# Performance work log

Hardware: AMD Instinct MI355X
Metric: run time of the kernel (lower is better)

## Reference

```python
import jax, jax.numpy as jnp
import numpy as np

# MXInt config (mirrors q_config in init_kwargs)
A_MW, A_EW = 8, 4   # matmul input A mantissa/exponent widths
B_MW, B_EW = 8, 4   # matmul input B
O_MW, O_EW = 8, 4   # matmul output
SM_MW, SM_EW = 8, 4 # softmax output


def _dequant(m, e, mw):
    # m: [..., S, D] integer-valued mantissas; e: [..., S] shared row exponent
    # value = m * 2^(e - mw + 1)
    return m * jnp.exp2(e.astype(m.dtype)[..., None] - (mw - 1))


def _quant(x, mw, ew):
    # MXInt block quantization with exponent shared over the last dim.
    amax = jnp.max(jnp.abs(x), axis=-1)
    e = jnp.floor(jnp.log2(jnp.maximum(amax, jnp.exp2(jnp.float32(-126)))))
    e = jnp.clip(e, -(2 ** (ew - 1)), 2 ** (ew - 1) - 1)
    m = jnp.round(x * jnp.exp2(-(e[..., None] - (mw - 1))))
    m = jnp.clip(m, -(2 ** (mw - 1)), 2 ** (mw - 1) - 1)
    return m, e


def setup_inputs() -> dict:
    key = jax.random.key(0)
    ks = jax.random.split(key, 6)
    B, S, D = 256, 512, 64
    mquery = jax.random.randint(ks[0], (B, S, D), 0, 128).astype(jnp.float32)
    mkey = jax.random.randint(ks[1], (B, S, D), 0, 128).astype(jnp.float32)
    mvalue = jax.random.randint(ks[2], (B, S, D), 0, 128).astype(jnp.float32)
    equery = jax.random.randint(ks[3], (B, S), 0, 6, dtype=jnp.int32)
    ekey = jax.random.randint(ks[4], (B, S), 0, 6, dtype=jnp.int32)
    evalue = jax.random.randint(ks[5], (B, S), 0, 6, dtype=jnp.int32)
    return {"mquery": mquery, "equery": equery, "mkey": mkey,
            "ekey": ekey, "mvalue": mvalue, "evalue": evalue}


def reference(mquery, equery, mkey, ekey, mvalue, evalue):
    # QK^T in dequantized domain, then requantize output to MXInt (per-row exp)
    q = _dequant(mquery, equery, A_MW)            # [B,S,D]
    k = _dequant(mkey, ekey, B_MW)                # [B,S,D]
    scores = jnp.einsum('bsd,btd->bst', q, k)     # [B,S,S]
    m_s, _e_s = _quant(scores, O_MW, O_EW)
    # Note: the torch module calls the softmax on the score MANTISSAS only
    # (the score exponent is dropped), then requantizes the probabilities.
    probs = jax.nn.softmax(m_s, axis=-1)
    m_p, e_p = _quant(probs, SM_MW, SM_EW)
    # AV matmul: dequant probs with A widths, values with B widths
    p = _dequant(m_p, e_p, A_MW)                  # [B,S,S]
    v = _dequant(mvalue, evalue, B_MW)            # [B,S,D]
    ctx = jnp.einsum('bst,btd->bsd', p, v)        # [B,S,D]
    m_c, e_c = _quant(ctx, O_MW, O_EW)
    # final dequant exactly as the module: m * 2^(e - OUT_MAN_WIDTH + 1)
    return m_c * jnp.exp2(e_c[..., None] - O_MW + 1)
```

## Files before the change

kernel.cpp:

```cpp
#include <hip/hip_runtime.h>
#include <math.h>

#define S_LEN 512
#define D_DIM 64

typedef __attribute__((ext_vector_type(8))) short bf16x8;
typedef __attribute__((ext_vector_type(4))) float f32x4;
typedef __attribute__((ext_vector_type(4))) unsigned int u32x4;
typedef unsigned int u32;
typedef unsigned long long u64;

__device__ __forceinline__ float pow2i(int e) {
    return __int_as_float((e + 127) << 23);
}
__device__ __forceinline__ u32 pack_bf2(float lo, float hi) {
    return __builtin_amdgcn_perm(__float_as_uint(hi), __float_as_uint(lo), 0x07060302u);
}

extern "C" __global__ void __launch_bounds__(512, 2)
mxattn(const float* __restrict__ gmq, const int* __restrict__ geq,
       const float* __restrict__ gmk, const int* __restrict__ gek,
       const float* __restrict__ gmv, const int* __restrict__ gev,
       float* __restrict__ gout)
{
    __shared__ __attribute__((aligned(16))) short Ksw[S_LEN * D_DIM];
    __shared__ __attribute__((aligned(16))) short Vsw[D_DIM * S_LEN];
    __shared__ __attribute__((aligned(16))) char Pex[8 * 2 * 64 * 16];

    const int b    = blockIdx.x;
    const int tid  = threadIdx.x;
    const int lane = tid & 63;
    const int wave = tid >> 6;
    const int l15  = lane & 15;
    const int lg   = lane >> 4;

    const float* mqb = gmq + (size_t)b * (S_LEN * D_DIM);
    const float* mkb = gmk + (size_t)b * (S_LEN * D_DIM);
    const float* mvb = gmv + (size_t)b * (S_LEN * D_DIM);
    const int* eqb = geq + b * S_LEN;
    const int* ekb = gek + b * S_LEN;
    const int* evb = gev + b * S_LEN;

    char* kbase = (char*)Ksw;
    char* vbase = (char*)Vsw;

    #pragma unroll
    for (int it = 0; it < 16; ++it) {
        int idx = it * 512 + tid;
        int t = idx >> 4, d0 = (idx & 15) * 4;
        float ks = pow2i(ekb[t] - 7);
        f32x4 mk4 = *(const f32x4*)(mkb + t * 64 + d0);
        u32 klo = pack_bf2(mk4[0] * ks, mk4[1] * ks);
        u32 khi = pack_bf2(mk4[2] * ks, mk4[3] * ks);
        *(u64*)(kbase + t * 128 + ((2 * d0) ^ ((t & 7) << 4))) = ((u64)khi << 32) | klo;
        float vs = pow2i(evb[t] - 7);
        f32x4 mv4 = *(const f32x4*)(mvb + t * 64 + d0);
        #pragma unroll
        for (int i = 0; i < 4; ++i) {
            int d = d0 + i;
            *(short*)(vbase + d * 1024 + ((2 * t) ^ ((d & 7) << 4))) =
                (short)(__float_as_uint(mv4[i] * vs) >> 16);
        }
    }
    float sqp[4];
    #pragma unroll
    for (int p = 0; p < 4; ++p) sqp[p] = pow2i(eqb[p * 128 + wave * 16 + l15] - 7);
    __syncthreads();

    const float L2E = 1.44269504088896340736f;
    const int p_ = lg >> 1;
    const int srcA = l15 + ((lg & 1) << 5);
    const int srcAoff = srcA * 16 + (p_ << 3);

    for (int pass = 0; pass < 4; ++pass) {
        const int r0 = pass * 128 + wave * 16;

        bf16x8 qa0, qa1;
        {
            const float* qp = mqb + (size_t)(r0 + l15) * 64 + lg * 8;
            f32x4 a0 = *(const f32x4*)(qp);
            f32x4 a1 = *(const f32x4*)(qp + 4);
            f32x4 a2 = *(const f32x4*)(qp + 32);
            f32x4 a3 = *(const f32x4*)(qp + 36);
            u32x4 q0 = { pack_bf2(a0[0], a0[1]), pack_bf2(a0[2], a0[3]),
                         pack_bf2(a1[0], a1[1]), pack_bf2(a1[2], a1[3]) };
            u32x4 q1 = { pack_bf2(a2[0], a2[1]), pack_bf2(a2[2], a2[3]),
                         pack_bf2(a3[0], a3[1]), pack_bf2(a3[2], a3[3]) };
            qa0 = *(bf16x8*)&q0;
            qa1 = *(bf16x8*)&q1;
        }

        f32x4 acc[32];
        #pragma unroll
        for (int tt = 0; tt < 32; ++tt) acc[tt] = f32x4{0.f, 0.f, 0.f, 0.f};
        #pragma unroll
        for (int tt = 0; tt < 32; ++tt) {
            int t = tt * 16 + l15;
            int row = t * 128, sw = (t & 7) << 4;
            bf16x8 kf0 = *(const bf16x8*)(kbase + row + ((16 * lg) ^ sw));
            bf16x8 kf1 = *(const bf16x8*)(kbase + row + ((64 + 16 * lg) ^ sw));
            acc[tt] = __builtin_amdgcn_mfma_f32_16x16x32_bf16(kf0, qa0, acc[tt], 0, 0, 0);
            acc[tt] = __builtin_amdgcn_mfma_f32_16x16x32_bf16(kf1, qa1, acc[tt], 0, 0, 0);
        }

        float am0 = 0.f, am1 = 0.f, am2 = 0.f, am3 = 0.f;
        #pragma unroll
        for (int tt = 0; tt < 32; ++tt) {
            am0 = fmaxf(am0, acc[tt][0]); am1 = fmaxf(am1, acc[tt][1]);
            am2 = fmaxf(am2, acc[tt][2]); am3 = fmaxf(am3, acc[tt][3]);
        }
        float amax = fmaxf(fmaxf(am0, am1), fmaxf(am2, am3));
        amax = fmaxf(amax, __shfl_xor(amax, 16));
        amax = fmaxf(amax, __shfl_xor(amax, 32));

        const float sq = sqp[pass];
        float as = fmaxf(amax * sq, 1.17549435e-38f);
        int es = (int)((__float_as_uint(as) >> 23) & 0xFFu) - 127;
        es = es < -8 ? -8 : (es > 7 ? 7 : es);
        const float c1 = sq * pow2i(7 - es);
        const float M = fminf(rintf(amax * c1), 127.f);
        const float nML2E = -M * L2E;

        float s0 = 0.f, s1 = 0.f, s2 = 0.f, s3 = 0.f;
        #pragma unroll
        for (int tt = 0; tt < 32; ++tt) {
            f32x4 a = acc[tt];
            float m0 = fminf(rintf(a[0] * c1), 127.f);
            float m1 = fminf(rintf(a[1] * c1), 127.f);
            float m2 = fminf(rintf(a[2] * c1), 127.f);
            float m3 = fminf(rintf(a[3] * c1), 127.f);
            a[0] = exp2f(fmaf(m0, L2E, nML2E));
            a[1] = exp2f(fmaf(m1, L2E, nML2E));
            a[2] = exp2f(fmaf(m2, L2E, nML2E));
            a[3] = exp2f(fmaf(m3, L2E, nML2E));
            s0 += a[0]; s1 += a[1]; s2 += a[2]; s3 += a[3];
            acc[tt] = a;
        }
        float sum = (s0 + s1) + (s2 + s3);
        sum += __shfl_xor(sum, 16);
        sum += __shfl_xor(sum, 32);

        float pm = fmaxf(1.0f / sum, 1.17549435e-38f);
        int ep = (int)((__float_as_uint(pm) >> 23) & 0xFFu) - 127;
        ep = ep < -8 ? -8 : (ep > 7 ? 7 : ep);
        const float sp = pow2i(7 - ep) / sum;
        const float osc = pow2i(ep - 7);

        f32x4 ctx[4];
        #pragma unroll
        for (int dt = 0; dt < 4; ++dt) ctx[dt] = f32x4{0.f, 0.f, 0.f, 0.f};
        #pragma unroll
        for (int c = 0; c < 16; ++c) {
            char* pb = Pex + (size_t)(wave * 2 + (c & 1)) * 1024;
            f32x4 aA = acc[2 * c], aB = acc[2 * c + 1];
            float m0 = fminf(rintf(aA[0] * sp), 127.f);
            float m1 = fminf(rintf(aA[1] * sp), 127.f);
            float m2 = fminf(rintf(aA[2] * sp), 127.f);
            float m3 = fminf(rintf(aA[3] * sp), 127.f);
            float m4 = fminf(rintf(aB[0] * sp), 127.f);
            float m5 = fminf(rintf(aB[1] * sp), 127.f);
            float m6 = fminf(rintf(aB[2] * sp), 127.f);
            float m7 = fminf(rintf(aB[3] * sp), 127.f);
            u32x4 wv = { pack_bf2(m0, m1), pack_bf2(m2, m3),
                         pack_bf2(m4, m5), pack_bf2(m6, m7) };
            *(u32x4*)(pb + lane * 16) = wv;
            asm volatile("s_waitcnt lgkmcnt(0)" ::: "memory");
            u64 pa = *(const u64*)(pb + srcAoff);
            u64 pc = *(const u64*)(pb + srcAoff + 256);
            union { u64 q[2]; bf16x8 h; } pu;
            pu.q[0] = pa; pu.q[1] = pc;
            bf16x8 pf = pu.h;
            int tbase = 2 * (c * 32 + 8 * lg);
            #pragma unroll
            for (int dt = 0; dt < 4; ++dt) {
                int d = dt * 16 + l15;
                bf16x8 vf = *(const bf16x8*)(vbase + d * 1024 + (tbase ^ ((d & 7) << 4)));
                ctx[dt] = __builtin_amdgcn_mfma_f32_16x16x32_bf16(pf, vf, ctx[dt], 0, 0, 0);
            }
        }

        float oscr[4];
        #pragma unroll
        for (int j = 0; j < 4; ++j) oscr[j] = __shfl(osc, lg * 4 + j);
        float cv[4][4];
        float a4[4] = {0.f, 0.f, 0.f, 0.f};
        #pragma unroll
        for (int dt = 0; dt < 4; ++dt)
            #pragma unroll
            for (int j = 0; j < 4; ++j) {
                float x = ctx[dt][j] * oscr[j];
                cv[dt][j] = x;
                a4[j] = fmaxf(a4[j], fabsf(x));
            }
        #pragma unroll
        for (int j = 0; j < 4; ++j) {
            #pragma unroll
            for (int off = 1; off < 16; off <<= 1)
                a4[j] = fmaxf(a4[j], __shfl_xor(a4[j], off));
        }
        float csc[4], oo[4];
        #pragma unroll
        for (int j = 0; j < 4; ++j) {
            float a = fmaxf(a4[j], 1.17549435e-38f);
            int ec = (int)((__float_as_uint(a) >> 23) & 0xFFu) - 127;
            ec = ec < -8 ? -8 : (ec > 7 ? 7 : ec);
            csc[j] = pow2i(7 - ec);
            oo[j] = pow2i(ec - 7);
        }
        #pragma unroll
        for (int dt = 0; dt < 4; ++dt)
            #pragma unroll
            for (int j = 0; j < 4; ++j) {
                float m = rintf(cv[dt][j] * csc[j]);
                m = fminf(fmaxf(m, -128.f), 127.f);
                gout[((size_t)b * S_LEN + r0 + lg * 4 + j) * D_DIM + dt * 16 + l15] = m * oo[j];
            }
    }
}

extern "C" void kernel_launch(void* const* d_in, const int* in_sizes, int n_in,
                              void* d_out, int out_size, void* d_ws, size_t ws_size,
                              hipStream_t stream) {
    const float* mq = (const float*)d_in[0];
    const int*   eq = (const int*)d_in[1];
    const float* mk = (const float*)d_in[2];
    const int*   ek = (const int*)d_in[3];
    const float* mv = (const float*)d_in[4];
    const int*   ev = (const int*)d_in[5];
    float* out = (float*)d_out;
    int B = in_sizes[1] / S_LEN;
    mxattn<<<B, 512, 0, stream>>>(mq, eq, mk, ek, mv, ev, out);
}
```

Before: 64.52 us.

## Store K and V in LDS in MFMA fragment order for linear lane reads

K and V are now written into shared memory already arranged as per-lane MFMA operand fragments, so the inner loops read 16 contiguous bytes per lane without XOR swizzle address math. V is transposed by having each lane gather eight strided global values and write one packed 16-byte store, replacing scattered 2-byte shared stores. The V exponent scales are first staged in a small shared table, which adds an extra barrier. The cost is uncoalesced, strided global reads of V during the fill, in exchange for cheaper, conflict-free shared reads in the hot loops.

```diff
diff --git a/kernel.cpp b/kernel.cpp
--- a/kernel.cpp
+++ b/kernel.cpp
@@ -23,9 +23,10 @@
        const float* __restrict__ gmv, const int* __restrict__ gev,
        float* __restrict__ gout)
 {
-    __shared__ __attribute__((aligned(16))) short Ksw[S_LEN * D_DIM];
-    __shared__ __attribute__((aligned(16))) short Vsw[D_DIM * S_LEN];
+    __shared__ __attribute__((aligned(16))) short Ktile[32768];
+    __shared__ __attribute__((aligned(16))) short Vtile[32768];
     __shared__ __attribute__((aligned(16))) char Pex[8 * 2 * 64 * 16];
+    __shared__ __attribute__((aligned(16))) float evtab[S_LEN];
 
     const int b    = blockIdx.x;
     const int tid  = threadIdx.x;
@@ -41,26 +42,45 @@
     const int* ekb = gek + b * S_LEN;
     const int* evb = gev + b * S_LEN;
 
-    char* kbase = (char*)Ksw;
-    char* vbase = (char*)Vsw;
-
+    char* kb = (char*)Ktile;
+    char* vb = (char*)Vtile;
+
+    evtab[tid] = pow2i(evb[tid] - 7);
     #pragma unroll
-    for (int it = 0; it < 16; ++it) {
-        int idx = it * 512 + tid;
-        int t = idx >> 4, d0 = (idx & 15) * 4;
+    for (int i = 0; i < 4; ++i) {
+        int tt = wave * 4 + i;
+        int t = tt * 16 + l15;
         float ks = pow2i(ekb[t] - 7);
-        f32x4 mk4 = *(const f32x4*)(mkb + t * 64 + d0);
-        u32 klo = pack_bf2(mk4[0] * ks, mk4[1] * ks);
-        u32 khi = pack_bf2(mk4[2] * ks, mk4[3] * ks);
-        *(u64*)(kbase + t * 128 + ((2 * d0) ^ ((t & 7) << 4))) = ((u64)khi << 32) | klo;
-        float vs = pow2i(evb[t] - 7);
-        f32x4 mv4 = *(const f32x4*)(mvb + t * 64 + d0);
-        #pragma unroll
-        for (int i = 0; i < 4; ++i) {
-            int d = d0 + i;
-            *(short*)(vbase + d * 1024 + ((2 * t) ^ ((d & 7) << 4))) =
-                (short)(__float_as_uint(mv4[i] * vs) >> 16);
-        }
+        const float* kp = mkb + t * 64 + lg * 8;
+        f32x4 a0 = *(const f32x4*)(kp);
+        f32x4 a1 = *(const f32x4*)(kp + 4);
+        f32x4 a2 = *(const f32x4*)(kp + 32);
+        f32x4 a3 = *(const f32x4*)(kp + 36);
+        u32x4 w0 = { pack_bf2(a0[0] * ks, a0[1] * ks), pack_bf2(a0[2] * ks, a0[3] * ks),
+                     pack_bf2(a1[0] * ks, a1[1] * ks), pack_bf2(a1[2] * ks, a1[3] * ks) };
+        u32x4 w1 = { pack_bf2(a2[0] * ks, a2[1] * ks), pack_bf2(a2[2] * ks, a2[3] * ks),
+                     pack_bf2(a3[0] * ks, a3[1] * ks), pack_bf2(a3[2] * ks, a3[3] * ks) };
+        *(u32x4*)(kb + tt * 2048 + lane * 16) = w0;
+        *(u32x4*)(kb + tt * 2048 + 1024 + lane * 16) = w1;
+    }
+    __syncthreads();
+
+    #pragma unroll
+    for (int i = 0; i < 8; ++i) {
+        int idx = wave * 8 + i;
+        int tb = (idx >> 2) * 32 + lg * 8;
+        int dcol = (idx & 3) * 16 + l15;
+        float v0 = mvb[(tb + 0) * 64 + dcol] * evtab[tb + 0];
+        float v1 = mvb[(tb + 1) * 64 + dcol] * evtab[tb + 1];
+        float v2 = mvb[(tb + 2) * 64 + dcol] * evtab[tb + 2];
+        float v3 = mvb[(tb + 3) * 64 + dcol] * evtab[tb + 3];
+        float v4 = mvb[(tb + 4) * 64 + dcol] * evtab[tb + 4];
+        float v5 = mvb[(tb + 5) * 64 + dcol] * evtab[tb + 5];
+        float v6 = mvb[(tb + 6) * 64 + dcol] * evtab[tb + 6];
+        float v7 = mvb[(tb + 7) * 64 + dcol] * evtab[tb + 7];
+        u32x4 wv = { pack_bf2(v0, v1), pack_bf2(v2, v3),
+                     pack_bf2(v4, v5), pack_bf2(v6, v7) };
+        *(u32x4*)(vb + idx * 1024 + lane * 16) = wv;
     }
     float sqp[4];
     #pragma unroll
@@ -95,10 +115,8 @@
         for (int tt = 0; tt < 32; ++tt) acc[tt] = f32x4{0.f, 0.f, 0.f, 0.f};
         #pragma unroll
         for (int tt = 0; tt < 32; ++tt) {
-            int t = tt * 16 + l15;
-            int row = t * 128, sw = (t & 7) << 4;
-            bf16x8 kf0 = *(const bf16x8*)(kbase + row + ((16 * lg) ^ sw));
-            bf16x8 kf1 = *(const bf16x8*)(kbase + row + ((64 + 16 * lg) ^ sw));
+            bf16x8 kf0 = *(const bf16x8*)(kb + tt * 2048 + lane * 16);
+            bf16x8 kf1 = *(const bf16x8*)(kb + tt * 2048 + 1024 + lane * 16);
             acc[tt] = __builtin_amdgcn_mfma_f32_16x16x32_bf16(kf0, qa0, acc[tt], 0, 0, 0);
             acc[tt] = __builtin_amdgcn_mfma_f32_16x16x32_bf16(kf1, qa1, acc[tt], 0, 0, 0);
         }
@@ -170,11 +188,9 @@
             union { u64 q[2]; bf16x8 h; } pu;
             pu.q[0] = pa; pu.q[1] = pc;
             bf16x8 pf = pu.h;
-            int tbase = 2 * (c * 32 + 8 * lg);
             #pragma unroll
             for (int dt = 0; dt < 4; ++dt) {
-                int d = dt * 16 + l15;
-                bf16x8 vf = *(const bf16x8*)(vbase + d * 1024 + (tbase ^ ((d & 7) << 4)));
+                bf16x8 vf = *(const bf16x8*)(vb + (c * 4 + dt) * 1024 + lane * 16);
                 ctx[dt] = __builtin_amdgcn_mfma_f32_16x16x32_bf16(pf, vf, ctx[dt], 0, 0, 0);
             }
         }
```

Result: no change. 65.03 us (+0.8%).
